# Performance work log

Hardware: AMD Instinct MI355X
Metric: run time of the kernel (lower is better)

## Reference

```python
import jax, jax.numpy as jnp
import numpy as np

N_NODES = 16384
N_EDGES = 65536
N_GRAPHS = 64


def setup_inputs() -> dict:
    key = jax.random.key(0)
    ks = iter(jax.random.split(key, 64))
    nk = lambda: next(ks)
    p = lambda *s: jax.random.normal(nk(), s, jnp.float32) * 0.1
    inp = {}
    inp['x'] = jax.random.normal(nk(), (N_NODES, 1), jnp.float32)
    inp['edge_index'] = jax.random.randint(nk(), (2, N_EDGES), 0, N_NODES, dtype=jnp.int32)
    inp['batch'] = jnp.sort(jax.random.randint(nk(), (N_NODES,), 0, N_GRAPHS, dtype=jnp.int32))
    for i, (fi, fo) in [(1, (1, 64)), (2, (64, 512)), (3, (512, 2048))]:
        inp[f'gat{i}_wl'] = p(fi, fo)
        inp[f'gat{i}_wr'] = p(fi, fo)
        inp[f'gat{i}_att'] = p(fo)
        inp[f'gat{i}_b'] = jnp.zeros((fo,), jnp.float32)
    for i, c in [(1, 64), (2, 512), (3, 2048), (4, 512), (5, 64)]:
        inp[f'gn{i}_w'] = jnp.ones((c,), jnp.float32)
        inp[f'gn{i}_b'] = jnp.zeros((c,), jnp.float32)
        inp[f'gn{i}_ms'] = jnp.ones((c,), jnp.float32)
    for i, (fi, fo) in [(1, (2048, 512)), (2, (512, 64))]:
        inp[f'arma{i}_wi'] = p(fi, fo)
        inp[f'arma{i}_wr'] = p(fi, fo)
        inp[f'arma{i}_b'] = jnp.zeros((fo,), jnp.float32)
    inp['lin_w'] = p(192, 2)
    inp['lin_b'] = jnp.zeros((2,), jnp.float32)
    return inp


def _seg_softmax(e, idx, n):
    m = jax.ops.segment_max(e, idx, num_segments=n)
    ex = jnp.exp(e - m[idx])
    s = jax.ops.segment_sum(ex, idx, num_segments=n)
    return ex / (s[idx] + 1e-16)


def _gatv2(x, src, dst, wl, wr, att, b):
    # GATv2: e_ij = a^T LeakyReLU(W_l x_j + W_r x_i), softmax over dst neighborhoods
    n = x.shape[0]
    xl = x @ wl
    xr = x @ wr
    e = jax.nn.leaky_relu(xl[src] + xr[dst], 0.2) @ att  # [E]
    a = _seg_softmax(e, dst, n)
    return jax.ops.segment_sum(xl[src] * a[:, None], dst, num_segments=n) + b


def _graph_norm(x, batch, w, b, ms, cnt):
    mean = jax.ops.segment_sum(x, batch, num_segments=N_GRAPHS) / cnt
    out = x - mean[batch] * ms
    var = jax.ops.segment_sum(out * out, batch, num_segments=N_GRAPHS) / cnt
    return w * out / jnp.sqrt(var + 1e-5)[batch] + b


def _arma(x, src, dst, norm, wi, wr, b):
    # ARMAConv, num_stacks=1, num_layers=1: ReLU(Ahat (x Wi) + x Wr + b)
    agg = jax.ops.segment_sum((x @ wi)[src] * norm[:, None], dst, num_segments=x.shape[0])
    return jax.nn.relu(agg + x @ wr + b)


def _forward(x, edge_index, batch,
             gat1_wl, gat1_wr, gat1_att, gat1_b, gn1_w, gn1_b, gn1_ms,
             gat2_wl, gat2_wr, gat2_att, gat2_b, gn2_w, gn2_b, gn2_ms,
             gat3_wl, gat3_wr, gat3_att, gat3_b, gn3_w, gn3_b, gn3_ms,
             arma1_wi, arma1_wr, arma1_b, gn4_w, gn4_b, gn4_ms,
             arma2_wi, arma2_wr, arma2_b, gn5_w, gn5_b, gn5_ms,
             lin_w, lin_b):
    n = x.shape[0]
    src, dst = edge_index[0], edge_index[1]
    sl = jnp.arange(n, dtype=edge_index.dtype)
    src_sl = jnp.concatenate([src, sl])  # GATv2 adds self loops
    dst_sl = jnp.concatenate([dst, sl])
    # gcn_norm without self loops (ARMAConv default)
    deg = jax.ops.segment_sum(jnp.ones_like(src, dtype=x.dtype), dst, num_segments=n)
    dis = jnp.where(deg > 0, 1.0 / jnp.sqrt(jnp.maximum(deg, 1.0)), 0.0)
    norm = dis[src] * dis[dst]
    cnt = jnp.maximum(jax.ops.segment_sum(jnp.ones((n,), x.dtype), batch, num_segments=N_GRAPHS), 1.0)[:, None]

    h = jax.nn.elu(_gatv2(x, src_sl, dst_sl, gat1_wl, gat1_wr, gat1_att, gat1_b))
    h = _graph_norm(h, batch, gn1_w, gn1_b, gn1_ms, cnt)
    h = jax.nn.elu(_gatv2(h, src_sl, dst_sl, gat2_wl, gat2_wr, gat2_att, gat2_b))
    h = _graph_norm(h, batch, gn2_w, gn2_b, gn2_ms, cnt)
    h = jax.nn.elu(_gatv2(h, src_sl, dst_sl, gat3_wl, gat3_wr, gat3_att, gat3_b))
    h = _graph_norm(h, batch, gn3_w, gn3_b, gn3_ms, cnt)
    h = jax.nn.elu(_arma(h, src, dst, norm, arma1_wi, arma1_wr, arma1_b))
    h = _graph_norm(h, batch, gn4_w, gn4_b, gn4_ms, cnt)
    h = jax.nn.elu(_arma(h, src, dst, norm, arma2_wi, arma2_wr, arma2_b))
    h = _graph_norm(h, batch, gn5_w, gn5_b, gn5_ms, cnt)

    x_max = jax.ops.segment_max(h, batch, num_segments=N_GRAPHS)
    x_sum = jax.ops.segment_sum(h, batch, num_segments=N_GRAPHS)
    x_mean = x_sum / cnt
    return jnp.concatenate([x_max, x_mean, x_sum], axis=1) @ lin_w + lin_b


def reference(x, edge_index, batch,
              gat1_wl, gat1_wr, gat1_att, gat1_b, gn1_w, gn1_b, gn1_ms,
              gat2_wl, gat2_wr, gat2_att, gat2_b, gn2_w, gn2_b, gn2_ms,
              gat3_wl, gat3_wr, gat3_att, gat3_b, gn3_w, gn3_b, gn3_ms,
              arma1_wi, arma1_wr, arma1_b, gn4_w, gn4_b, gn4_ms,
              arma2_wi, arma2_wr, arma2_b, gn5_w, gn5_b, gn5_ms,
              lin_w, lin_b):
    return _forward(x, edge_index, batch,
                    gat1_wl, gat1_wr, gat1_att, gat1_b, gn1_w, gn1_b, gn1_ms,
                    gat2_wl, gat2_wr, gat2_att, gat2_b, gn2_w, gn2_b, gn2_ms,
                    gat3_wl, gat3_wr, gat3_att, gat3_b, gn3_w, gn3_b, gn3_ms,
                    arma1_wi, arma1_wr, arma1_b, gn4_w, gn4_b, gn4_ms,
                    arma2_wi, arma2_wr, arma2_b, gn5_w, gn5_b, gn5_ms,
                    lin_w, lin_b)
```

## Files before the change

kernel.cpp:

```cpp
#include <hip/hip_runtime.h>
#include <hip/hip_bf16.h>

#define NN 16384
#define NE 65536
#define NESL (NE + NN)
#define NG 64

typedef __hip_bfloat16 bf16;
typedef __attribute__((ext_vector_type(8))) short short8v;
typedef __attribute__((ext_vector_type(4))) float f32x4;
typedef __attribute__((address_space(3))) void lds_void;
typedef const __attribute__((address_space(1))) void glb_void;

__device__ __forceinline__ short bfbits(float v) {
  bf16 h = __float2bfloat16(v);
  return *(short*)&h;
}
__device__ __forceinline__ float bfs2f(short s) {
  return __uint_as_float(((unsigned)(unsigned short)s) << 16);
}
__device__ __forceinline__ void gld16(const void* g, void* l) {
  __builtin_amdgcn_global_load_lds((glb_void*)g, (lds_void*)l, 16, 0, 0);
}

__global__ void k_zero2(int* a, int* b, int n) {
  int i = blockIdx.x * blockDim.x + threadIdx.x;
  if (i < n) { a[i] = 0; b[i] = 0; }
}


__global__ void k_ranges(const int* __restrict__ batch, int* __restrict__ R,
                         float* __restrict__ cnt) {
  int g = threadIdx.x;
  if (g <= NG) {
    int lo = 0, hi = NN;
    while (lo < hi) { int mid = (lo + hi) >> 1; if (batch[mid] < g) lo = mid + 1; else hi = mid; }
    R[g] = lo;
  }
  __syncthreads();
  if (g < NG) cnt[g] = fmaxf((float)(R[g + 1] - R[g]), 1.0f);
}

__global__ void k_deg(const int* __restrict__ dst, int* __restrict__ deg) {
  int e = blockIdx.x * blockDim.x + threadIdx.x;
  if (e < NE) atomicAdd(deg + dst[e], 1);
}

__global__ void k_dis(const int* __restrict__ deg, float* __restrict__ dis) {
  int n = blockIdx.x * blockDim.x + threadIdx.x;
  if (n < NN) { int d = deg[n]; dis[n] = d > 0 ? 1.0f / sqrtf((float)d) : 0.0f; }
}

__global__ void k_scan(const int* __restrict__ deg, int* __restrict__ rowptr) {
  __shared__ int sums[1024];
  int tid = threadIdx.x;
  int base = tid * 16;
  int loc[16];
  int run = 0;
#pragma unroll
  for (int i = 0; i < 16; i++) { run += deg[base + i] + 1; loc[i] = run; }
  sums[tid] = run;
  __syncthreads();
  for (int off = 1; off < 1024; off <<= 1) {
    int v = sums[tid];
    int u = (tid >= off) ? sums[tid - off] : 0;
    __syncthreads();
    sums[tid] = v + u;
    __syncthreads();
  }
  int offset = (tid > 0) ? sums[tid - 1] : 0;
  if (tid == 0) rowptr[0] = 0;
#pragma unroll
  for (int i = 0; i < 16; i++) rowptr[base + i + 1] = loc[i] + offset;
}

__global__ void k_fill(const int* __restrict__ src, const int* __restrict__ dst,
                       const int* __restrict__ rowptr, const float* __restrict__ dis,
                       int* __restrict__ fill, int* __restrict__ srck,
                       float* __restrict__ normk) {
  int e = blockIdx.x * blockDim.x + threadIdx.x;
  if (e >= NESL) return;
  int s = e < NE ? src[e] : e - NE;
  int d = e < NE ? dst[e] : e - NE;
  int pos = rowptr[d] + atomicAdd(fill + d, 1);
  srck[pos] = s;
  normk[pos] = e < NE ? dis[s] * dis[d] : 0.0f;
}

__device__ __forceinline__ size_t pidx(int n, int k, int K) {
  size_t t = (size_t)(n >> 7) * (K >> 5) + (k >> 5);
  int col = n & 127, kk = k & 31;
  int lane = ((kk >> 3) << 4) | (col & 15);
  return t * 4096 + (size_t)((col >> 4) * 512 + lane * 8 + (kk & 7));
}

__global__ void k_wsplit_pk(const float* __restrict__ w, short* __restrict__ hi,
                            short* __restrict__ lo, int K, int N, int n0) {
  int i = blockIdx.x * blockDim.x + threadIdx.x;
  if (i >= N * K) return;
  int n = i / K, k = i % K;
  float v = w[(size_t)k * N + n];
  short h = bfbits(v);
  size_t pi = pidx(n0 + n, k, K);
  hi[pi] = h;
  lo[pi] = bfbits(v - bfs2f(h));
}

__device__ __forceinline__ int swz(int row, int kbyte) {
  return ((row << 6) + kbyte) ^ ((row & 7) << 4);
}

__device__ __forceinline__ void splitw2(const float* ap, char* hidst, char* lodst) {
  f32x4 va = *(const f32x4*)ap;
  f32x4 vb = *(const f32x4*)(ap + 4);
  float f[8] = {va[0], va[1], va[2], va[3], vb[0], vb[1], vb[2], vb[3]};
  short8v h, l;
#pragma unroll
  for (int j = 0; j < 8; j++) {
    short hb = bfbits(f[j]);
    h[j] = hb;
    l[j] = bfbits(f[j] - bfs2f(hb));
  }
  *(short8v*)hidst = h;
  *(short8v*)lodst = l;
}

template <int CBF16, int ACT>
__global__ __launch_bounds__(256) void gemm_mfma_s(const float* __restrict__ Ap,
                                                   const short* __restrict__ Bthi,
                                                   const short* __restrict__ Btlo,
                                                   void* __restrict__ Cp,
                                                   const float* __restrict__ bias,
                                                   int M, int N, int K) {
  __shared__ __align__(16) short sAhi[128 * 32];
  __shared__ __align__(16) short sAlo[128 * 32];
  __shared__ __align__(16) short sBhi[128 * 32];
  __shared__ __align__(16) short sBlo[128 * 32];
  const int tid = threadIdx.x;
  const int wave = tid >> 6, lane = tid & 63;
  const int wm = wave >> 1, wn = wave & 1;
  const int row0 = blockIdx.y * 128, col0 = blockIdx.x * 128;
  const int lr = lane & 15;
  const int lkb = (lane >> 4) * 16;
  const int nkb = K >> 5;
  f32x4 acc[4][4] = {};

  for (int kb = 0; kb < nkb; kb++) {
    {
      const short* bh = Bthi + ((size_t)(col0 >> 7) * nkb + kb) * 4096;
      const short* bl = Btlo + ((size_t)(col0 >> 7) * nkb + kb) * 4096;
      int c = wave * 2;
      gld16(bh + (size_t)c * 512 + lane * 8, (char*)sBhi + c * 1024);
      gld16(bh + (size_t)(c + 1) * 512 + lane * 8, (char*)sBhi + (c + 1) * 1024);
      gld16(bl + (size_t)c * 512 + lane * 8, (char*)sBlo + c * 1024);
      gld16(bl + (size_t)(c + 1) * 512 + lane * 8, (char*)sBlo + (c + 1) * 1024);
    }
    {
      int r = tid >> 1, kbf = (tid & 1) * 16;
      const float* ap = Ap + (size_t)(row0 + r) * K + kb * 32 + kbf;
      int b0 = swz(r, kbf * 2), b1 = swz(r, kbf * 2 + 16);
      splitw2(ap, (char*)sAhi + b0, (char*)sAlo + b0);
      splitw2(ap + 8, (char*)sAhi + b1, (char*)sAlo + b1);
    }
    __syncthreads();
    short8v af[4], al[4], bh[4], bl[4];
#pragma unroll
    for (int f = 0; f < 4; f++) {
      int b = swz(wm * 64 + f * 16 + lr, lkb);
      af[f] = *(short8v*)((char*)sAhi + b);
      al[f] = *(short8v*)((char*)sAlo + b);
      int b2 = (wn * 4 + f) * 1024 + lane * 16;
      bh[f] = *(short8v*)((char*)sBhi + b2);
      bl[f] = *(short8v*)((char*)sBlo + b2);
    }
#pragma unroll
    for (int i = 0; i < 4; i++)
#pragma unroll
      for (int j = 0; j < 4; j++) {
        acc[i][j] = __builtin_amdgcn_mfma_f32_16x16x32_bf16(af[i], bh[j], acc[i][j], 0, 0, 0);
        acc[i][j] = __builtin_amdgcn_mfma_f32_16x16x32_bf16(af[i], bl[j], acc[i][j], 0, 0, 0);
        acc[i][j] = __builtin_amdgcn_mfma_f32_16x16x32_bf16(al[i], bh[j], acc[i][j], 0, 0, 0);
      }
    __syncthreads();
  }
#pragma unroll
  for (int i = 0; i < 4; i++)
#pragma unroll
    for (int j = 0; j < 4; j++)
#pragma unroll
      for (int r = 0; r < 4; r++) {
        int row = row0 + wm * 64 + i * 16 + ((lane >> 4) << 2) + r;
        int col = col0 + wn * 64 + j * 16 + lr;
        float v = acc[i][j][r];
        if (bias) v += bias[col];
        if constexpr (ACT == 1) v = v > 0.0f ? v : expf(v) - 1.0f;
        if constexpr (ACT == 2) v = fmaxf(v, 0.0f);
        if constexpr (CBF16) {
          ((short*)Cp)[(size_t)row * N + col] = bfbits(v);
        } else {
          ((float*)Cp)[(size_t)row * N + col] = v;
        }
      }
}

template <int CBF16, int ACT>
__global__ __launch_bounds__(256) void gemm_mfma_p(const short* __restrict__ A,
                                                   const short* __restrict__ Bthi,
                                                   const short* __restrict__ Btlo,
                                                   void* __restrict__ Cp,
                                                   const float* __restrict__ bias,
                                                   int M, int N, int K) {
  __shared__ __align__(16) short sA[2][4096];
  __shared__ __align__(16) short sB[2][8192];
  const int tid = threadIdx.x;
  const int wave = tid >> 6, lane = tid & 63;
  const int wm = wave >> 1, wn = wave & 1;
  const int row0 = blockIdx.y * 128, col0 = blockIdx.x * 128;
  const int nkb = K >> 5;
  const int c = wave * 2;
  const int ar = lane & 15, akc = lane >> 4;
  f32x4 acc[4][4] = {};

  auto stage = [&](int buf, int kb) {
    const short* bh = Bthi + ((size_t)(col0 >> 7) * nkb + kb) * 4096;
    const short* bl = Btlo + ((size_t)(col0 >> 7) * nkb + kb) * 4096;
    gld16(bh + (size_t)c * 512 + lane * 8, (char*)sB[buf] + c * 1024);
    gld16(bh + (size_t)(c + 1) * 512 + lane * 8, (char*)sB[buf] + (c + 1) * 1024);
    gld16(bl + (size_t)c * 512 + lane * 8, (char*)sB[buf] + 8192 + c * 1024);
    gld16(bl + (size_t)(c + 1) * 512 + lane * 8, (char*)sB[buf] + 8192 + (c + 1) * 1024);
    gld16(A + (size_t)(row0 + c * 16 + ar) * K + kb * 32 + akc * 8,
          (char*)sA[buf] + c * 1024);
    gld16(A + (size_t)(row0 + (c + 1) * 16 + ar) * K + kb * 32 + akc * 8,
          (char*)sA[buf] + (c + 1) * 1024);
  };

  stage(0, 0);
  for (int kb = 0; kb < nkb; kb++) {
    int cur = kb & 1;
    if (kb + 1 < nkb) {
      stage(cur ^ 1, kb + 1);
      asm volatile("s_waitcnt vmcnt(6)" ::: "memory");
    } else {
      asm volatile("s_waitcnt vmcnt(0)" ::: "memory");
    }
    __builtin_amdgcn_s_barrier();
    short8v af[4], bh[4], bl[4];
#pragma unroll
    for (int f = 0; f < 4; f++) {
      af[f] = *(short8v*)((char*)sA[cur] + (wm * 4 + f) * 1024 + lane * 16);
      bh[f] = *(short8v*)((char*)sB[cur] + (wn * 4 + f) * 1024 + lane * 16);
      bl[f] = *(short8v*)((char*)sB[cur] + 8192 + (wn * 4 + f) * 1024 + lane * 16);
    }
#pragma unroll
    for (int i = 0; i < 4; i++)
#pragma unroll
      for (int j = 0; j < 4; j++) {
        acc[i][j] = __builtin_amdgcn_mfma_f32_16x16x32_bf16(af[i], bh[j], acc[i][j], 0, 0, 0);
        acc[i][j] = __builtin_amdgcn_mfma_f32_16x16x32_bf16(af[i], bl[j], acc[i][j], 0, 0, 0);
      }
    __builtin_amdgcn_s_barrier();
  }
#pragma unroll
  for (int i = 0; i < 4; i++)
#pragma unroll
    for (int j = 0; j < 4; j++)
#pragma unroll
      for (int r = 0; r < 4; r++) {
        int row = row0 + wm * 64 + i * 16 + ((lane >> 4) << 2) + r;
        int col = col0 + wn * 64 + j * 16 + (lane & 15);
        float v = acc[i][j][r];
        if (bias) v += bias[col];
        if constexpr (ACT == 1) v = v > 0.0f ? v : expf(v) - 1.0f;
        if constexpr (ACT == 2) v = fmaxf(v, 0.0f);
        if constexpr (CBF16) {
          ((short*)Cp)[(size_t)row * N + col] = bfbits(v);
        } else {
          ((float*)Cp)[(size_t)row * N + col] = v;
        }
      }
}

__global__ void k_gat1_csr(const float* __restrict__ x, const float* __restrict__ wl,
                           const float* __restrict__ wr, const float* __restrict__ att,
                           const int* __restrict__ rowptr, const int* __restrict__ srck,
                           float* __restrict__ ework, const float* __restrict__ bias,
                           float* __restrict__ out) {
  int node = blockIdx.x * 4 + (threadIdx.x >> 6);
  int lane = threadIdx.x & 63;
  float wlv = wl[lane], wrv = wr[lane], av = att[lane];
  float xd = x[node];
  int beg = rowptr[node], end = rowptr[node + 1];
  float m = -INFINITY;
  for (int k = beg; k < end; k++) {
    float v = x[srck[k]] * wlv + xd * wrv;
    v = v > 0.0f ? v : 0.2f * v;
    float e = av * v;
#pragma unroll
    for (int off = 32; off; off >>= 1) e += __shfl_xor(e, off);
    if (lane == 0) ework[k] = e;
    m = fmaxf(m, e);
  }
  __syncthreads();
  float sum = 0.0f, agg = 0.0f;
  for (int k = beg + lane; k < end; k += 64) {
    float p = expf(ework[k] - m);
    sum += p;
    agg += p * x[srck[k]];
  }
#pragma unroll
  for (int off = 32; off; off >>= 1) {
    sum += __shfl_xor(sum, off);
    agg += __shfl_xor(agg, off);
  }
  float o = agg / (sum + 1e-16f) * wlv + bias[lane];
  out[(size_t)node * 64 + lane] = o > 0.0f ? o : expf(o) - 1.0f;
}

template <int FO, int STR, typename XT>
__global__ void k_logits_csr(const XT* __restrict__ X, const float* __restrict__ att,
                             const int* __restrict__ rowptr, const int* __restrict__ srck,
                             float* __restrict__ pk, float* __restrict__ ssum) {
  int node = blockIdx.x * 4 + (threadIdx.x >> 6);
  int lane = threadIdx.x & 63;
  constexpr int NV = FO / 64;
  float xr[NV], at[NV];
  if constexpr (sizeof(XT) == 2) {
    const short* xrp = (const short*)X + (size_t)node * STR + FO;
#pragma unroll
    for (int j = 0; j < FO / 512; j++) {
      short8v v = *(const short8v*)(xrp + j * 512 + lane * 8);
      f32x4 a0 = *(const f32x4*)(att + j * 512 + lane * 8);
      f32x4 a1 = *(const f32x4*)(att + j * 512 + lane * 8 + 4);
#pragma unroll
      for (int t = 0; t < 8; t++) {
        xr[j * 8 + t] = bfs2f(v[t]);
        at[j * 8 + t] = t < 4 ? a0[t] : a1[t - 4];
      }
    }
  } else {
    const float* xrp = (const float*)X + (size_t)node * STR + FO;
#pragma unroll
    for (int j = 0; j < FO / 256; j++) {
      f32x4 v = *(const f32x4*)(xrp + j * 256 + lane * 4);
      f32x4 a = *(const f32x4*)(att + j * 256 + lane * 4);
#pragma unroll
      for (int t = 0; t < 4; t++) {
        xr[j * 4 + t] = v[t];
        at[j * 4 + t] = a[t];
      }
    }
  }
  int beg = rowptr[node], end = rowptr[node + 1];
  float m = -INFINITY;
  for (int k = beg; k < end; k++) {
    int s = srck[k];
    float acc = 0.0f;
    if constexpr (sizeof(XT) == 2) {
      const short* xlp = (const short*)X + (size_t)s * STR;
#pragma unroll
      for (int j = 0; j < FO / 512; j++) {
        short8v v = *(const short8v*)(xlp + j * 512 + lane * 8);
#pragma unroll
        for (int t = 0; t < 8; t++) {
          float u = bfs2f(v[t]) + xr[j * 8 + t];
          u = u > 0.0f ? u : 0.2f * u;
          acc += at[j * 8 + t] * u;
        }
      }
    } else {
      const float* xlp = (const float*)X + (size_t)s * STR;
#pragma unroll
      for (int j = 0; j < FO / 256; j++) {
        f32x4 v = *(const f32x4*)(xlp + j * 256 + lane * 4);
#pragma unroll
        for (int t = 0; t < 4; t++) {
          float u = v[t] + xr[j * 4 + t];
          u = u > 0.0f ? u : 0.2f * u;
          acc += at[j * 4 + t] * u;
        }
      }
    }
#pragma unroll
    for (int off = 32; off; off >>= 1) acc += __shfl_xor(acc, off);
    if (lane == 0) pk[k] = acc;
    m = fmaxf(m, acc);
  }
  __syncthreads();
  float sum = 0.0f;
  for (int k = beg + lane; k < end; k += 64) {
    float p = expf(pk[k] - m);
    pk[k] = p;
    sum += p;
  }
#pragma unroll
  for (int off = 32; off; off >>= 1) sum += __shfl_xor(sum, off);
  if (lane == 0) ssum[node] = sum;
}

template <int MODE, int SSTR, int OSTR>
__global__ void k_agg512(const float* __restrict__ Xsrc, const float* __restrict__ pk,
                         const float* __restrict__ ssum, const int* __restrict__ rowptr,
                         const int* __restrict__ srck, const float* __restrict__ normk,
                         const float* __restrict__ xwrb, const float* __restrict__ bias,
                         float* __restrict__ out) {
  int wave = threadIdx.x >> 6;
  int node = blockIdx.x * 2 + (wave >> 1);
  int lane = threadIdx.x & 63;
  int c0 = (wave & 1) * 256 + lane * 4;
  f32x4 acc = {};
  int beg = rowptr[node], end = rowptr[node + 1];
  float inv = (MODE == 0) ? 1.0f / (ssum[node] + 1e-16f) : 1.0f;
  for (int k = beg; k < end; k++) {
    int s = srck[k];
    float w = (MODE == 0) ? pk[k] * inv : normk[k];
    f32x4 v = *(const f32x4*)(Xsrc + (size_t)s * SSTR + c0);
#pragma unroll
    for (int t = 0; t < 4; t++) acc[t] += w * v[t];
  }
  if constexpr (MODE == 1) {
    f32x4 xv = *(const f32x4*)(xwrb + (size_t)node * SSTR + 512 + c0);
#pragma unroll
    for (int t = 0; t < 4; t++) acc[t] = fmaxf(acc[t] + xv[t] + bias[c0 + t], 0.0f);
  }
  *(f32x4*)(out + (size_t)node * OSTR + c0) = acc;
}

template <int MODE, int SSTR, int XOFF>
__global__ void k_agg64(const float* __restrict__ Xsrc, const float* __restrict__ pk,
                        const float* __restrict__ ssum, const int* __restrict__ rowptr,
                        const int* __restrict__ srck, const float* __restrict__ normk,
                        const float* __restrict__ xwrb, const float* __restrict__ bias,
                        float* __restrict__ out) {
  int node = blockIdx.x * (blockDim.x >> 6) + (threadIdx.x >> 6);
  if (node >= NN) return;
  int lane = threadIdx.x & 63;
  int cg = lane & 15, eg = lane >> 4;
  int c0 = cg * 4;
  f32x4 acc = {};
  int beg = rowptr[node], end = rowptr[node + 1];
  float inv = (MODE == 0) ? 1.0f / (ssum[node] + 1e-16f) : 1.0f;
  for (int k = beg + eg; k < end; k += 4) {
    int s = srck[k];
    float w = (MODE == 0) ? pk[k] * inv : normk[k];
    f32x4 v = *(const f32x4*)(Xsrc + (size_t)s * SSTR + c0);
#pragma unroll
    for (int t = 0; t < 4; t++) acc[t] += w * v[t];
  }
#pragma unroll
  for (int t = 0; t < 4; t++) {
    acc[t] += __shfl_xor(acc[t], 16);
    acc[t] += __shfl_xor(acc[t], 32);
  }
  if (eg == 0) {
    if constexpr (MODE == 1) {
      f32x4 xv = *(const f32x4*)(xwrb + (size_t)node * SSTR + XOFF + c0);
#pragma unroll
      for (int t = 0; t < 4; t++) acc[t] = fmaxf(acc[t] + xv[t] + bias[c0 + t], 0.0f);
    }
    *(f32x4*)(out + (size_t)node * 64 + c0) = acc;
  }
}

template <typename T, int VEC>
__global__ void k_gn_stats_v(const T* __restrict__ x, const int* __restrict__ R, int C,
                             float* __restrict__ s1, float* __restrict__ s2) {
  int g = blockIdx.x;
  int c0 = (blockIdx.y * blockDim.x + threadIdx.x) * VEC;
  if (c0 >= C) return;
  int beg = R[g], end = R[g + 1];
  float a[VEC] = {}, b[VEC] = {};
  for (int n = beg; n < end; n++) {
    const T* p = x + (size_t)n * C + c0;
    float v[VEC];
    if constexpr (sizeof(T) == 2) {
      short8v h = *(const short8v*)p;
#pragma unroll
      for (int t = 0; t < VEC; t++) v[t] = bfs2f(h[t]);
    } else {
      f32x4 h = *(const f32x4*)p;
#pragma unroll
      for (int t = 0; t < VEC; t++) v[t] = h[t];
    }
#pragma unroll
    for (int t = 0; t < VEC; t++) {
      a[t] += v[t];
      b[t] += v[t] * v[t];
    }
  }
#pragma unroll
  for (int t = 0; t < VEC; t++) {
    s1[g * C + c0 + t] = a[t];
    s2[g * C + c0 + t] = b[t];
  }
}

template <typename T, int VEC, int EMIT>
__global__ void k_gn_apply_v(T* __restrict__ x, const int* __restrict__ batch,
                             const float* __restrict__ cnt, const float* __restrict__ s1,
                             const float* __restrict__ s2, const float* __restrict__ w,
                             const float* __restrict__ b, const float* __restrict__ ms, int C,
                             int total_vec, short* __restrict__ hip) {
  int i = blockIdx.x * blockDim.x + threadIdx.x;
  if (i >= total_vec) return;
  int cpv = C / VEC;
  int n = i / cpv, c0 = (i % cpv) * VEC;
  int g = batch[n];
  float ct = cnt[g];
  T* p = x + (size_t)n * C + c0;
  float v[VEC];
  if constexpr (sizeof(T) == 2) {
    short8v h = *(const short8v*)p;
#pragma unroll
    for (int t = 0; t < VEC; t++) v[t] = bfs2f(h[t]);
  } else {
    f32x4 h = *(const f32x4*)p;
#pragma unroll
    for (int t = 0; t < VEC; t++) v[t] = h[t];
  }
#pragma unroll
  for (int t = 0; t < VEC; t++) {
    int cc = c0 + t;
    float mean = s1[g * C + cc] / ct;
    float mm = mean * ms[cc];
    float var = s2[g * C + cc] / ct - 2.0f * mm * mean + mm * mm;
    v[t] = (v[t] - mm) * (1.0f / sqrtf(var + 1e-5f)) * w[cc] + b[cc];
  }
  if constexpr (sizeof(T) == 2) {
    short8v h;
#pragma unroll
    for (int t = 0; t < VEC; t++) h[t] = bfbits(v[t]);
    *(short8v*)p = h;
  } else {
    f32x4 h;
#pragma unroll
    for (int t = 0; t < VEC; t++) h[t] = v[t];
    *(f32x4*)p = h;
  }
  if constexpr (EMIT == 2) {
    typedef __attribute__((ext_vector_type(4))) short short4v;
    short4v hh;
#pragma unroll
    for (int t = 0; t < VEC; t++) hh[t] = bfbits(v[t]);
    *(short4v*)(hip + (size_t)n * C + c0) = hh;
  }
}

__global__ void k_pool(const float* __restrict__ h, const int* __restrict__ R,
                       const float* __restrict__ cnt, const float* __restrict__ lw,
                       const float* __restrict__ lb, float* __restrict__ out) {
  int g = blockIdx.x;
  int c = threadIdx.x;
  int beg = R[g], end = R[g + 1];
  float mx = -INFINITY, sm = 0.0f;
  for (int n = beg; n < end; n++) {
    float v = h[(size_t)n * 64 + c];
    mx = fmaxf(mx, v);
    sm += v;
  }
  __shared__ float feat[192];
  feat[c] = mx;
  feat[64 + c] = sm / cnt[g];
  feat[128 + c] = sm;
  __syncthreads();
  if (c < 2) {
    float acc = lb[c];
    for (int j = 0; j < 192; j++) acc += feat[j] * lw[j * 2 + c];
    out[g * 2 + c] = acc;
  }
}


extern "C" void kernel_launch(void* const* d_in, const int* in_sizes, int n_in,
                              void* d_out, int out_size, void* d_ws, size_t ws_size,
                              hipStream_t stream) {
  const float* x = (const float*)d_in[0];
  const int* ei = (const int*)d_in[1];
  const int* batch = (const int*)d_in[2];
  const float* g1wl = (const float*)d_in[3];
  const float* g1wr = (const float*)d_in[4];
  const float* g1att = (const float*)d_in[5];
  const float* g1b = (const float*)d_in[6];
  const float* g2wl = (const float*)d_in[7];
  const float* g2wr = (const float*)d_in[8];
  const float* g2att = (const float*)d_in[9];
  const float* g2b = (const float*)d_in[10];
  const float* g3wl = (const float*)d_in[11];
  const float* g3wr = (const float*)d_in[12];
  const float* g3att = (const float*)d_in[13];
  const float* g3b = (const float*)d_in[14];
  const float* gn1w = (const float*)d_in[15];
  const float* gn1b = (const float*)d_in[16];
  const float* gn1ms = (const float*)d_in[17];
  const float* gn2w = (const float*)d_in[18];
  const float* gn2b = (const float*)d_in[19];
  const float* gn2ms = (const float*)d_in[20];
  const float* gn3w = (const float*)d_in[21];
  const float* gn3b = (const float*)d_in[22];
  const float* gn3ms = (const float*)d_in[23];
  const float* gn4w = (const float*)d_in[24];
  const float* gn4b = (const float*)d_in[25];
  const float* gn4ms = (const float*)d_in[26];
  const float* gn5w = (const float*)d_in[27];
  const float* gn5b = (const float*)d_in[28];
  const float* gn5ms = (const float*)d_in[29];
  const float* a1wi = (const float*)d_in[30];
  const float* a1wr = (const float*)d_in[31];
  const float* a1b = (const float*)d_in[32];
  const float* a2wi = (const float*)d_in[33];
  const float* a2wr = (const float*)d_in[34];
  const float* a2b = (const float*)d_in[35];
  const float* linw = (const float*)d_in[36];
  const float* linb = (const float*)d_in[37];
  const int* srcp = ei;
  const int* dstp = ei + NE;
  float* out = (float*)d_out;

  float* ws = (float*)d_ws;
  size_t o = 0;
  auto alloc = [&](size_t nfloats) { float* p = ws + o; o += nfloats; return p; };
  float* BIG0f = alloc((size_t)NN * 1024);
  float* BIG1f = alloc((size_t)NN * 1024);
  float* B0 = alloc((size_t)NN * 512);
  float* B1 = alloc((size_t)NN * 512);
  float* h1 = alloc((size_t)NN * 64);
  float* aggS = alloc((size_t)NN * 64);
  float* S0 = alloc((size_t)NN * 64);
  float* S1 = alloc((size_t)NN * 64);
  float* S2 = alloc((size_t)NN * 64);
  float* pk = alloc(NESL);
  float* normk = alloc(NESL);
  float* ssum = alloc(NN);
  float* dis = alloc(NN);
  float* cnt = alloc(NG);
  float* s1 = alloc(NG * 2048);
  float* s2 = alloc(NG * 2048);
  short* WThi = (short*)alloc((size_t)4096 * 512 / 2);
  short* WTlo = (short*)alloc((size_t)4096 * 512 / 2);
  int* deg = (int*)alloc(NN);
  int* rowptr = (int*)alloc(NN + 1);
  int* fill = (int*)alloc(NN);
  int* srck = (int*)alloc(NESL);
  int* R = (int*)alloc(72);

  bf16* XLR3 = (bf16*)BIG0f;
  bf16* h3 = (bf16*)BIG0f;
  float* h4 = BIG1f;
  float* XLR2 = B0;
  float* h2 = B0;
  short* h2hi = (short*)B1;
  float* agg2 = B1;
  float* TXW1 = B0;
  float* TXW2 = S0;

  k_zero2<<<NN / 256, 256, 0, stream>>>(deg, fill, NN);
  k_ranges<<<1, 128, 0, stream>>>(batch, R, cnt);
  k_deg<<<NE / 256, 256, 0, stream>>>(dstp, deg);
  k_scan<<<1, 1024, 0, stream>>>(deg, rowptr);
  k_dis<<<NN / 256, 256, 0, stream>>>(deg, dis);
  k_fill<<<(NESL + 255) / 256, 256, 0, stream>>>(srcp, dstp, rowptr, dis, fill, srck, normk);

  k_gat1_csr<<<NN / 4, 256, 0, stream>>>(x, g1wl, g1wr, g1att, rowptr, srck, pk, g1b, h1);
  k_gn_stats_v<float, 4><<<dim3(NG, 1), 16, 0, stream>>>(h1, R, 64, s1, s2);
  k_gn_apply_v<float, 4, 0><<<NN * 16 / 256, 256, 0, stream>>>(h1, batch, cnt, s1, s2, gn1w,
                                                               gn1b, gn1ms, 64, NN * 16, nullptr);

  k_wsplit_pk<<<(512 * 64 + 255) / 256, 256, 0, stream>>>(g2wl, WThi, WTlo, 64, 512, 0);
  k_wsplit_pk<<<(512 * 64 + 255) / 256, 256, 0, stream>>>(g2wr, WThi, WTlo, 64, 512, 512);
  gemm_mfma_s<0, 0><<<dim3(8, 128), 256, 0, stream>>>(h1, WThi, WTlo, XLR2, nullptr, NN, 1024, 64);
  k_logits_csr<512, 1024, float><<<NN / 4, 256, 0, stream>>>(XLR2, g2att, rowptr, srck, pk, ssum);
  k_agg64<0, 64, 0><<<NN / 4, 256, 0, stream>>>(h1, pk, ssum, rowptr, srck, normk, nullptr,
                                                nullptr, aggS);
  gemm_mfma_s<0, 1><<<dim3(4, 128), 256, 0, stream>>>(aggS, WThi, WTlo, h2, g2b, NN, 512, 64);
  k_gn_stats_v<float, 4><<<dim3(NG, 1), 128, 0, stream>>>(h2, R, 512, s1, s2);
  k_gn_apply_v<float, 4, 2><<<NN * 128 / 256, 256, 0, stream>>>(h2, batch, cnt, s1, s2, gn2w,
                                                                gn2b, gn2ms, 512, NN * 128, h2hi);

  k_wsplit_pk<<<(2048 * 512 + 255) / 256, 256, 0, stream>>>(g3wl, WThi, WTlo, 512, 2048, 0);
  k_wsplit_pk<<<(2048 * 512 + 255) / 256, 256, 0, stream>>>(g3wr, WThi, WTlo, 512, 2048, 2048);
  gemm_mfma_p<1, 0><<<dim3(32, 128), 256, 0, stream>>>(h2hi, WThi, WTlo, XLR3, nullptr, NN,
                                                       4096, 512);
  k_logits_csr<2048, 4096, bf16><<<NN / 4, 256, 0, stream>>>(XLR3, g3att, rowptr, srck, pk, ssum);
  k_agg512<0, 512, 512><<<NN / 2, 256, 0, stream>>>(h2, pk, ssum, rowptr, srck, normk, nullptr,
                                                    nullptr, agg2);
  gemm_mfma_s<1, 1><<<dim3(16, 128), 256, 0, stream>>>(agg2, WThi, WTlo, h3, g3b, NN, 2048, 512);
  k_gn_stats_v<bf16, 8><<<dim3(NG, 1), 256, 0, stream>>>(h3, R, 2048, s1, s2);
  k_gn_apply_v<bf16, 8, 0><<<NN * 256 / 256, 256, 0, stream>>>(h3, batch, cnt, s1, s2, gn3w,
                                                               gn3b, gn3ms, 2048, NN * 256,
                                                               nullptr);

  k_wsplit_pk<<<(512 * 2048 + 255) / 256, 256, 0, stream>>>(a1wi, WThi, WTlo, 2048, 512, 0);
  k_wsplit_pk<<<(512 * 2048 + 255) / 256, 256, 0, stream>>>(a1wr, WThi, WTlo, 2048, 512, 512);
  gemm_mfma_p<0, 0><<<dim3(8, 128), 256, 0, stream>>>((const short*)h3, WThi, WTlo, TXW1,
                                                      nullptr, NN, 1024, 2048);
  k_agg512<1, 1024, 512><<<NN / 2, 256, 0, stream>>>(TXW1, pk, nullptr, rowptr, srck, normk,
                                                     TXW1, a1b, h4);
  k_gn_stats_v<float, 4><<<dim3(NG, 1), 128, 0, stream>>>(h4, R, 512, s1, s2);
  k_gn_apply_v<float, 4, 0><<<NN * 128 / 256, 256, 0, stream>>>(h4, batch, cnt, s1, s2, gn4w,
                                                                gn4b, gn4ms, 512, NN * 128,
                                                                nullptr);

  k_wsplit_pk<<<(64 * 512 + 255) / 256, 256, 0, stream>>>(a2wi, WThi, WTlo, 512, 64, 0);
  k_wsplit_pk<<<(64 * 512 + 255) / 256, 256, 0, stream>>>(a2wr, WThi, WTlo, 512, 64, 64);
  gemm_mfma_s<0, 0><<<dim3(1, 128), 256, 0, stream>>>(h4, WThi, WTlo, TXW2, nullptr, NN, 128, 512);
  k_agg64<1, 128, 64><<<NN / 4, 256, 0, stream>>>(TXW2, pk, nullptr, rowptr, srck, normk, TXW2,
                                                  a2b, S2);
  k_gn_stats_v<float, 4><<<dim3(NG, 1), 16, 0, stream>>>(S2, R, 64, s1, s2);
  k_gn_apply_v<float, 4, 0><<<NN * 16 / 256, 256, 0, stream>>>(S2, batch, cnt, s1, s2, gn5w,
                                                               gn5b, gn5ms, 64, NN * 16, nullptr);

  k_pool<<<NG, 64, 0, stream>>>(S2, R, cnt, linw, linb, out);
}
```

Before: 1.303 ms.

## Pre-split fp32 activations into bf16 hi/lo in producers, use pipelined GEMM

The single-buffered gemm_mfma_s, which split fp32 A tiles into bf16 hi/lo inside the main loop, is removed. The upstream producers (graph-norm apply and the aggregation kernels) now write hi/lo bf16 pairs directly, and every GEMM uses the double-buffered, async global-to-LDS gemm_mfma_p with an optional lo-A operand. This is meant to remove the in-loop conversion work and gain load/compute overlap. The cost is extra global writes and reads of the lo half, more LDS per block, and sched_barrier fences added around the barriers.

```diff
diff --git a/kernel.cpp b/kernel.cpp
--- a/kernel.cpp
+++ b/kernel.cpp
@@ -8,6 +8,7 @@
 
 typedef __hip_bfloat16 bf16;
 typedef __attribute__((ext_vector_type(8))) short short8v;
+typedef __attribute__((ext_vector_type(4))) short short4v;
 typedef __attribute__((ext_vector_type(4))) float f32x4;
 typedef __attribute__((address_space(3))) void lds_void;
 typedef const __attribute__((address_space(1))) void glb_void;
@@ -106,111 +107,15 @@
   lo[pi] = bfbits(v - bfs2f(h));
 }
 
-__device__ __forceinline__ int swz(int row, int kbyte) {
-  return ((row << 6) + kbyte) ^ ((row & 7) << 4);
-}
-
-__device__ __forceinline__ void splitw2(const float* ap, char* hidst, char* lodst) {
-  f32x4 va = *(const f32x4*)ap;
-  f32x4 vb = *(const f32x4*)(ap + 4);
-  float f[8] = {va[0], va[1], va[2], va[3], vb[0], vb[1], vb[2], vb[3]};
-  short8v h, l;
-#pragma unroll
-  for (int j = 0; j < 8; j++) {
-    short hb = bfbits(f[j]);
-    h[j] = hb;
-    l[j] = bfbits(f[j] - bfs2f(hb));
-  }
-  *(short8v*)hidst = h;
-  *(short8v*)lodst = l;
-}
-
-template <int CBF16, int ACT>
-__global__ __launch_bounds__(256) void gemm_mfma_s(const float* __restrict__ Ap,
+template <int SPLITA, int CBF16, int ACT>
+__global__ __launch_bounds__(256) void gemm_mfma_p(const short* __restrict__ Ahi,
+                                                   const short* __restrict__ Alo,
                                                    const short* __restrict__ Bthi,
                                                    const short* __restrict__ Btlo,
                                                    void* __restrict__ Cp,
                                                    const float* __restrict__ bias,
                                                    int M, int N, int K) {
-  __shared__ __align__(16) short sAhi[128 * 32];
-  __shared__ __align__(16) short sAlo[128 * 32];
-  __shared__ __align__(16) short sBhi[128 * 32];
-  __shared__ __align__(16) short sBlo[128 * 32];
-  const int tid = threadIdx.x;
-  const int wave = tid >> 6, lane = tid & 63;
-  const int wm = wave >> 1, wn = wave & 1;
-  const int row0 = blockIdx.y * 128, col0 = blockIdx.x * 128;
-  const int lr = lane & 15;
-  const int lkb = (lane >> 4) * 16;
-  const int nkb = K >> 5;
-  f32x4 acc[4][4] = {};
-
-  for (int kb = 0; kb < nkb; kb++) {
-    {
-      const short* bh = Bthi + ((size_t)(col0 >> 7) * nkb + kb) * 4096;
-      const short* bl = Btlo + ((size_t)(col0 >> 7) * nkb + kb) * 4096;
-      int c = wave * 2;
-      gld16(bh + (size_t)c * 512 + lane * 8, (char*)sBhi + c * 1024);
-      gld16(bh + (size_t)(c + 1) * 512 + lane * 8, (char*)sBhi + (c + 1) * 1024);
-      gld16(bl + (size_t)c * 512 + lane * 8, (char*)sBlo + c * 1024);
-      gld16(bl + (size_t)(c + 1) * 512 + lane * 8, (char*)sBlo + (c + 1) * 1024);
-    }
-    {
-      int r = tid >> 1, kbf = (tid & 1) * 16;
-      const float* ap = Ap + (size_t)(row0 + r) * K + kb * 32 + kbf;
-      int b0 = swz(r, kbf * 2), b1 = swz(r, kbf * 2 + 16);
-      splitw2(ap, (char*)sAhi + b0, (char*)sAlo + b0);
-      splitw2(ap + 8, (char*)sAhi + b1, (char*)sAlo + b1);
-    }
-    __syncthreads();
-    short8v af[4], al[4], bh[4], bl[4];
-#pragma unroll
-    for (int f = 0; f < 4; f++) {
-      int b = swz(wm * 64 + f * 16 + lr, lkb);
-      af[f] = *(short8v*)((char*)sAhi + b);
-      al[f] = *(short8v*)((char*)sAlo + b);
-      int b2 = (wn * 4 + f) * 1024 + lane * 16;
-      bh[f] = *(short8v*)((char*)sBhi + b2);
-      bl[f] = *(short8v*)((char*)sBlo + b2);
-    }
-#pragma unroll
-    for (int i = 0; i < 4; i++)
-#pragma unroll
-      for (int j = 0; j < 4; j++) {
-        acc[i][j] = __builtin_amdgcn_mfma_f32_16x16x32_bf16(af[i], bh[j], acc[i][j], 0, 0, 0);
-        acc[i][j] = __builtin_amdgcn_mfma_f32_16x16x32_bf16(af[i], bl[j], acc[i][j], 0, 0, 0);
-        acc[i][j] = __builtin_amdgcn_mfma_f32_16x16x32_bf16(al[i], bh[j], acc[i][j], 0, 0, 0);
-      }
-    __syncthreads();
-  }
-#pragma unroll
-  for (int i = 0; i < 4; i++)
-#pragma unroll
-    for (int j = 0; j < 4; j++)
-#pragma unroll
-      for (int r = 0; r < 4; r++) {
-        int row = row0 + wm * 64 + i * 16 + ((lane >> 4) << 2) + r;
-        int col = col0 + wn * 64 + j * 16 + lr;
-        float v = acc[i][j][r];
-        if (bias) v += bias[col];
-        if constexpr (ACT == 1) v = v > 0.0f ? v : expf(v) - 1.0f;
-        if constexpr (ACT == 2) v = fmaxf(v, 0.0f);
-        if constexpr (CBF16) {
-          ((short*)Cp)[(size_t)row * N + col] = bfbits(v);
-        } else {
-          ((float*)Cp)[(size_t)row * N + col] = v;
-        }
-      }
-}
-
-template <int CBF16, int ACT>
-__global__ __launch_bounds__(256) void gemm_mfma_p(const short* __restrict__ A,
-                                                   const short* __restrict__ Bthi,
-                                                   const short* __restrict__ Btlo,
-                                                   void* __restrict__ Cp,
-                                                   const float* __restrict__ bias,
-                                                   int M, int N, int K) {
-  __shared__ __align__(16) short sA[2][4096];
+  __shared__ __align__(16) short sA[2][(SPLITA ? 2 : 1) * 4096];
   __shared__ __align__(16) short sB[2][8192];
   const int tid = threadIdx.x;
   const int wave = tid >> 6, lane = tid & 63;
@@ -228,10 +133,16 @@
     gld16(bh + (size_t)(c + 1) * 512 + lane * 8, (char*)sB[buf] + (c + 1) * 1024);
     gld16(bl + (size_t)c * 512 + lane * 8, (char*)sB[buf] + 8192 + c * 1024);
     gld16(bl + (size_t)(c + 1) * 512 + lane * 8, (char*)sB[buf] + 8192 + (c + 1) * 1024);
-    gld16(A + (size_t)(row0 + c * 16 + ar) * K + kb * 32 + akc * 8,
+    gld16(Ahi + (size_t)(row0 + c * 16 + ar) * K + kb * 32 + akc * 8,
           (char*)sA[buf] + c * 1024);
-    gld16(A + (size_t)(row0 + (c + 1) * 16 + ar) * K + kb * 32 + akc * 8,
+    gld16(Ahi + (size_t)(row0 + (c + 1) * 16 + ar) * K + kb * 32 + akc * 8,
           (char*)sA[buf] + (c + 1) * 1024);
+    if constexpr (SPLITA) {
+      gld16(Alo + (size_t)(row0 + c * 16 + ar) * K + kb * 32 + akc * 8,
+            (char*)sA[buf] + 8192 + c * 1024);
+      gld16(Alo + (size_t)(row0 + (c + 1) * 16 + ar) * K + kb * 32 + akc * 8,
+            (char*)sA[buf] + 8192 + (c + 1) * 1024);
+    }
   };
 
   stage(0, 0);
@@ -239,15 +150,23 @@
     int cur = kb & 1;
     if (kb + 1 < nkb) {
       stage(cur ^ 1, kb + 1);
-      asm volatile("s_waitcnt vmcnt(6)" ::: "memory");
+      if constexpr (SPLITA)
+        asm volatile("s_waitcnt vmcnt(8)" ::: "memory");
+      else
+        asm volatile("s_waitcnt vmcnt(6)" ::: "memory");
     } else {
       asm volatile("s_waitcnt vmcnt(0)" ::: "memory");
     }
+    __builtin_amdgcn_sched_barrier(0);
     __builtin_amdgcn_s_barrier();
-    short8v af[4], bh[4], bl[4];
+    __builtin_amdgcn_sched_barrier(0);
+    asm volatile("" ::: "memory");
+    short8v af[4], al[4], bh[4], bl[4];
 #pragma unroll
     for (int f = 0; f < 4; f++) {
       af[f] = *(short8v*)((char*)sA[cur] + (wm * 4 + f) * 1024 + lane * 16);
+      if constexpr (SPLITA)
+        al[f] = *(short8v*)((char*)sA[cur] + 8192 + (wm * 4 + f) * 1024 + lane * 16);
       bh[f] = *(short8v*)((char*)sB[cur] + (wn * 4 + f) * 1024 + lane * 16);
       bl[f] = *(short8v*)((char*)sB[cur] + 8192 + (wn * 4 + f) * 1024 + lane * 16);
     }
@@ -257,8 +176,13 @@
       for (int j = 0; j < 4; j++) {
         acc[i][j] = __builtin_amdgcn_mfma_f32_16x16x32_bf16(af[i], bh[j], acc[i][j], 0, 0, 0);
         acc[i][j] = __builtin_amdgcn_mfma_f32_16x16x32_bf16(af[i], bl[j], acc[i][j], 0, 0, 0);
+        if constexpr (SPLITA)
+          acc[i][j] = __builtin_amdgcn_mfma_f32_16x16x32_bf16(al[i], bh[j], acc[i][j], 0, 0, 0);
       }
+    asm volatile("" ::: "memory");
+    __builtin_amdgcn_sched_barrier(0);
     __builtin_amdgcn_s_barrier();
+    __builtin_amdgcn_sched_barrier(0);
   }
 #pragma unroll
   for (int i = 0; i < 4; i++)
@@ -402,7 +326,8 @@
                          const float* __restrict__ ssum, const int* __restrict__ rowptr,
                          const int* __restrict__ srck, const float* __restrict__ normk,
                          const float* __restrict__ xwrb, const float* __restrict__ bias,
-                         float* __restrict__ out) {
+                         float* __restrict__ out, short* __restrict__ outhi,
+                         short* __restrict__ outlo) {
   int wave = threadIdx.x >> 6;
   int node = blockIdx.x * 2 + (wave >> 1);
   int lane = threadIdx.x & 63;
@@ -421,8 +346,17 @@
     f32x4 xv = *(const f32x4*)(xwrb + (size_t)node * SSTR + 512 + c0);
 #pragma unroll
     for (int t = 0; t < 4; t++) acc[t] = fmaxf(acc[t] + xv[t] + bias[c0 + t], 0.0f);
-  }
-  *(f32x4*)(out + (size_t)node * OSTR + c0) = acc;
+    *(f32x4*)(out + (size_t)node * OSTR + c0) = acc;
+  } else {
+    short4v hh, ll;
+#pragma unroll
+    for (int t = 0; t < 4; t++) {
+      hh[t] = bfbits(acc[t]);
+      ll[t] = bfbits(acc[t] - bfs2f(hh[t]));
+    }
+    *(short4v*)(outhi + (size_t)node * OSTR + c0) = hh;
+    *(short4v*)(outlo + (size_t)node * OSTR + c0) = ll;
+  }
 }
 
 template <int MODE, int SSTR, int XOFF>
@@ -430,7 +364,8 @@
                         const float* __restrict__ ssum, const int* __restrict__ rowptr,
                         const int* __restrict__ srck, const float* __restrict__ normk,
                         const float* __restrict__ xwrb, const float* __restrict__ bias,
-                        float* __restrict__ out) {
+                        float* __restrict__ out, short* __restrict__ outhi,
+                        short* __restrict__ outlo) {
   int node = blockIdx.x * (blockDim.x >> 6) + (threadIdx.x >> 6);
   if (node >= NN) return;
   int lane = threadIdx.x & 63;
@@ -456,8 +391,17 @@
       f32x4 xv = *(const f32x4*)(xwrb + (size_t)node * SSTR + XOFF + c0);
 #pragma unroll
       for (int t = 0; t < 4; t++) acc[t] = fmaxf(acc[t] + xv[t] + bias[c0 + t], 0.0f);
-    }
-    *(f32x4*)(out + (size_t)node * 64 + c0) = acc;
+      *(f32x4*)(out + (size_t)node * 64 + c0) = acc;
+    } else {
+      short4v hh, ll;
+#pragma unroll
+      for (int t = 0; t < 4; t++) {
+        hh[t] = bfbits(acc[t]);
+        ll[t] = bfbits(acc[t] - bfs2f(hh[t]));
+      }
+      *(short4v*)(outhi + (size_t)node * 64 + c0) = hh;
+      *(short4v*)(outlo + (size_t)node * 64 + c0) = ll;
+    }
   }
 }
 
@@ -499,7 +443,8 @@
                              const float* __restrict__ cnt, const float* __restrict__ s1,
                              const float* __restrict__ s2, const float* __restrict__ w,
                              const float* __restrict__ b, const float* __restrict__ ms, int C,
-                             int total_vec, short* __restrict__ hip) {
+                             int total_vec, short* __restrict__ hip,
+                             short* __restrict__ lop) {
   int i = blockIdx.x * blockDim.x + threadIdx.x;
   if (i >= total_vec) return;
   int cpv = C / VEC;
@@ -536,12 +481,17 @@
     for (int t = 0; t < VEC; t++) h[t] = v[t];
     *(f32x4*)p = h;
   }
-  if constexpr (EMIT == 2) {
-    typedef __attribute__((ext_vector_type(4))) short short4v;
+  if constexpr (EMIT >= 2) {
     short4v hh;
 #pragma unroll
     for (int t = 0; t < VEC; t++) hh[t] = bfbits(v[t]);
     *(short4v*)(hip + (size_t)n * C + c0) = hh;
+    if constexpr (EMIT == 3) {
+      short4v ll;
+#pragma unroll
+      for (int t = 0; t < VEC; t++) ll[t] = bfbits(v[t] - bfs2f(hh[t]));
+      *(short4v*)(lop + (size_t)n * C + c0) = ll;
+    }
   }
 }
 
@@ -623,7 +573,6 @@
   float* B0 = alloc((size_t)NN * 512);
   float* B1 = alloc((size_t)NN * 512);
   float* h1 = alloc((size_t)NN * 64);
-  float* aggS = alloc((size_t)NN * 64);
   float* S0 = alloc((size_t)NN * 64);
   float* S1 = alloc((size_t)NN * 64);
   float* S2 = alloc((size_t)NN * 64);
@@ -645,12 +594,20 @@
   bf16* XLR3 = (bf16*)BIG0f;
   bf16* h3 = (bf16*)BIG0f;
   float* h4 = BIG1f;
+  short* h4hi = (short*)BIG0f;
+  short* h4lo = h4hi + (size_t)NN * 512;
   float* XLR2 = B0;
   float* h2 = B0;
   short* h2hi = (short*)B1;
-  float* agg2 = B1;
+  short* agg2hi = (short*)B1;
+  short* agg2lo = agg2hi + (size_t)NN * 512;
   float* TXW1 = B0;
   float* TXW2 = S0;
+  short* h1hi = (short*)S2;
+  short* h1lo = h1hi + (size_t)NN * 64;
+  short* aggShi = (short*)S0;
+  short* aggSlo = aggShi + (size_t)NN * 64;
+  float* h5 = S2;
 
   k_zero2<<<NN / 256, 256, 0, stream>>>(deg, fill, NN);
   k_ranges<<<1, 128, 0, stream>>>(batch, R, cnt);
@@ -661,52 +618,59 @@
 
   k_gat1_csr<<<NN / 4, 256, 0, stream>>>(x, g1wl, g1wr, g1att, rowptr, srck, pk, g1b, h1);
   k_gn_stats_v<float, 4><<<dim3(NG, 1), 16, 0, stream>>>(h1, R, 64, s1, s2);
-  k_gn_apply_v<float, 4, 0><<<NN * 16 / 256, 256, 0, stream>>>(h1, batch, cnt, s1, s2, gn1w,
-                                                               gn1b, gn1ms, 64, NN * 16, nullptr);
+  k_gn_apply_v<float, 4, 3><<<NN * 16 / 256, 256, 0, stream>>>(h1, batch, cnt, s1, s2, gn1w,
+                                                               gn1b, gn1ms, 64, NN * 16, h1hi,
+                                                               h1lo);
 
   k_wsplit_pk<<<(512 * 64 + 255) / 256, 256, 0, stream>>>(g2wl, WThi, WTlo, 64, 512, 0);
   k_wsplit_pk<<<(512 * 64 + 255) / 256, 256, 0, stream>>>(g2wr, WThi, WTlo, 64, 512, 512);
-  gemm_mfma_s<0, 0><<<dim3(8, 128), 256, 0, stream>>>(h1, WThi, WTlo, XLR2, nullptr, NN, 1024, 64);
+  gemm_mfma_p<1, 0, 0><<<dim3(8, 128), 256, 0, stream>>>(h1hi, h1lo, WThi, WTlo, XLR2, nullptr,
+                                                         NN, 1024, 64);
   k_logits_csr<512, 1024, float><<<NN / 4, 256, 0, stream>>>(XLR2, g2att, rowptr, srck, pk, ssum);
   k_agg64<0, 64, 0><<<NN / 4, 256, 0, stream>>>(h1, pk, ssum, rowptr, srck, normk, nullptr,
-                                                nullptr, aggS);
-  gemm_mfma_s<0, 1><<<dim3(4, 128), 256, 0, stream>>>(aggS, WThi, WTlo, h2, g2b, NN, 512, 64);
+                                                nullptr, nullptr, aggShi, aggSlo);
+  gemm_mfma_p<1, 0, 1><<<dim3(4, 128), 256, 0, stream>>>(aggShi, aggSlo, WThi, WTlo, h2, g2b,
+                                                         NN, 512, 64);
   k_gn_stats_v<float, 4><<<dim3(NG, 1), 128, 0, stream>>>(h2, R, 512, s1, s2);
   k_gn_apply_v<float, 4, 2><<<NN * 128 / 256, 256, 0, stream>>>(h2, batch, cnt, s1, s2, gn2w,
-                                                                gn2b, gn2ms, 512, NN * 128, h2hi);
+                                                                gn2b, gn2ms, 512, NN * 128,
+                                                                h2hi, nullptr);
 
   k_wsplit_pk<<<(2048 * 512 + 255) / 256, 256, 0, stream>>>(g3wl, WThi, WTlo, 512, 2048, 0);
   k_wsplit_pk<<<(2048 * 512 + 255) / 256, 256, 0, stream>>>(g3wr, WThi, WTlo, 512, 2048, 2048);
-  gemm_mfma_p<1, 0><<<dim3(32, 128), 256, 0, stream>>>(h2hi, WThi, WTlo, XLR3, nullptr, NN,
-                                                       4096, 512);
+  gemm_mfma_p<0, 1, 0><<<dim3(32, 128), 256, 0, stream>>>(h2hi, nullptr, WThi, WTlo, XLR3,
+                                                          nullptr, NN, 4096, 512);
   k_logits_csr<2048, 4096, bf16><<<NN / 4, 256, 0, stream>>>(XLR3, g3att, rowptr, srck, pk, ssum);
   k_agg512<0, 512, 512><<<NN / 2, 256, 0, stream>>>(h2, pk, ssum, rowptr, srck, normk, nullptr,
-                                                    nullptr, agg2);
-  gemm_mfma_s<1, 1><<<dim3(16, 128), 256, 0, stream>>>(agg2, WThi, WTlo, h3, g3b, NN, 2048, 512);
+                                                    nullptr, nullptr, agg2hi, agg2lo);
+  gemm_mfma_p<1, 1, 1><<<dim3(16, 128), 256, 0, stream>>>(agg2hi, agg2lo, WThi, WTlo, h3, g3b,
+                                                          NN, 2048, 512);
   k_gn_stats_v<bf16, 8><<<dim3(NG, 1), 256, 0, stream>>>(h3, R, 2048, s1, s2);
   k_gn_apply_v<bf16, 8, 0><<<NN * 256 / 256, 256, 0, stream>>>(h3, batch, cnt, s1, s2, gn3w,
                                                                gn3b, gn3ms, 2048, NN * 256,
-                                                               nullptr);
+                                                               nullptr, nullptr);
 
   k_wsplit_pk<<<(512 * 2048 + 255) / 256, 256, 0, stream>>>(a1wi, WThi, WTlo, 2048, 512, 0);
   k_wsplit_pk<<<(512 * 2048 + 255) / 256, 256, 0, stream>>>(a1wr, WThi, WTlo, 2048, 512, 512);
-  gemm_mfma_p<0, 0><<<dim3(8, 128), 256, 0, stream>>>((const short*)h3, WThi, WTlo, TXW1,
-                                                      nullptr, NN, 1024, 2048);
+  gemm_mfma_p<0, 0, 0><<<dim3(8, 128), 256, 0, stream>>>((const short*)h3, nullptr, WThi, WTlo,
+                                                         TXW1, nullptr, NN, 1024, 2048);
   k_agg512<1, 1024, 512><<<NN / 2, 256, 0, stream>>>(TXW1, pk, nullptr, rowptr, srck, normk,
-                                                     TXW1, a1b, h4);
+                                                     TXW1, a1b, h4, nullptr, nullptr);
   k_gn_stats_v<float, 4><<<dim3(NG, 1), 128, 0, stream>>>(h4, R, 512, s1, s2);
-  k_gn_apply_v<float, 4, 0><<<NN * 128 / 256, 256, 0, stream>>>(h4, batch, cnt, s1, s2, gn4w,
+  k_gn_apply_v<float, 4, 3><<<NN * 128 / 256, 256, 0, stream>>>(h4, batch, cnt, s1, s2, gn4w,
                                                                 gn4b, gn4ms, 512, NN * 128,
-                                                                nullptr);
+                                                                h4hi, h4lo);
 
   k_wsplit_pk<<<(64 * 512 + 255) / 256, 256, 0, stream>>>(a2wi, WThi, WTlo, 512, 64, 0);
   k_wsplit_pk<<<(64 * 512 + 255) / 256, 256, 0, stream>>>(a2wr, WThi, WTlo, 512, 64, 64);
-  gemm_mfma_s<0, 0><<<dim3(1, 128), 256, 0, stream>>>(h4, WThi, WTlo, TXW2, nullptr, NN, 128, 512);
+  gemm_mfma_p<1, 0, 0><<<dim3(1, 128), 256, 0, stream>>>(h4hi, h4lo, WThi, WTlo, TXW2, nullptr,
+                                                         NN, 128, 512);
   k_agg64<1, 128, 64><<<NN / 4, 256, 0, stream>>>(TXW2, pk, nullptr, rowptr, srck, normk, TXW2,
-                                                  a2b, S2);
-  k_gn_stats_v<float, 4><<<dim3(NG, 1), 16, 0, stream>>>(S2, R, 64, s1, s2);
-  k_gn_apply_v<float, 4, 0><<<NN * 16 / 256, 256, 0, stream>>>(S2, batch, cnt, s1, s2, gn5w,
-                                                               gn5b, gn5ms, 64, NN * 16, nullptr);
-
-  k_pool<<<NG, 64, 0, stream>>>(S2, R, cnt, linw, linb, out);
-}
+                                                  a2b, h5, nullptr, nullptr);
+  k_gn_stats_v<float, 4><<<dim3(NG, 1), 16, 0, stream>>>(h5, R, 64, s1, s2);
+  k_gn_apply_v<float, 4, 0><<<NN * 16 / 256, 256, 0, stream>>>(h5, batch, cnt, s1, s2, gn5w,
+                                                               gn5b, gn5ms, 64, NN * 16, nullptr,
+                                                               nullptr);
+
+  k_pool<<<NG, 64, 0, stream>>>(h5, R, cnt, linw, linb, out);
+}
```

Result: no change. 1.317 ms (+1.0%).
